# Kernel optimization log

Hardware: AMD Instinct MI355X
Metric: run time of the kernel (lower is better)

## Reference

```python
import jax, jax.numpy as jnp
import numpy as np

B, N, F_TOT, F_OBS = 64, 128, 80, 64
TAU, THRESH, EPS = 1.0, 0.5, 1e-8


def setup_inputs() -> dict:
    key = jax.random.key(0)
    k1, k2 = jax.random.split(key)
    h = jax.random.normal(k1, (B, N, F_TOT), dtype=jnp.float32)
    # xavier_uniform with gain=1.414 for a_link of shape (F_OBS, 1)
    bound = 1.414 * np.sqrt(6.0 / (F_OBS + 1))
    a_link = jax.random.uniform(k2, (F_OBS, 1), dtype=jnp.float32, minval=-bound, maxval=bound)
    return {"h": h, "a_link": a_link, "rollout": 1}


def reference(h, a_link, rollout):
    # h is detached in the original forward
    h_obs = jax.lax.stop_gradient(h[:, :, :F_OBS])            # [B, N, F_OBS]
    # pairwise |h_i - h_j| projected to a scalar logit per edge
    diff = jnp.abs(h_obs[:, :, None, :] - h_obs[:, None, :, :])  # [B, N, N, F_OBS]
    logits = jnp.einsum('bijk,kl->bijl', diff, a_link)[..., 0]   # [B, N, N]
    # gumbel_sigmoid with rollout=True: no noise, hard threshold + straight-through
    y_soft = jax.nn.sigmoid(logits / TAU)
    y_hard = (y_soft > THRESH).astype(y_soft.dtype)
    A = y_hard - jax.lax.stop_gradient(y_soft) + y_soft
    # log-likelihood of the sampled off-diagonal adjacency entries
    selected = A * y_soft + (1.0 - A) * (1.0 - y_soft)
    offdiag = 1.0 - jnp.eye(N, dtype=y_soft.dtype)              # [N, N]
    probs = jnp.sum(jnp.log(selected + EPS) * offdiag[None], axis=(1, 2))  # [B]
    # zero the diagonal of A, then add identity (self-loops forced to 1)
    A = A * offdiag[None] + jnp.eye(N, dtype=A.dtype)[None]
    return A, probs
```

## Files before the change

kernel.cpp:

```cpp
#include <hip/hip_runtime.h>

#define GB 64
#define GN 128
#define F_OBS 64
#define F_TOT 80
#define ISPLIT 32
#define IPB (GN / ISPLIT)

__global__ __launch_bounds__(128, 4) void glcn_main(
    const float* __restrict__ h, const float* __restrict__ w,
    float* __restrict__ Aout, float* __restrict__ part) {
  const int blk = blockIdx.x;
  const int b  = (blk & 7) + 8 * ((blk >> 3) & 7);
  const int q  = blk >> 6;
  const int is = q * IPB;
  const int j  = threadIdx.x;

  const float* rowj = h + ((size_t)(b * GN + j)) * F_TOT;
  const float* rows = h + ((size_t)(b * GN + is)) * F_TOT;

  float4 hj[F_OBS / 4];
#pragma unroll
  for (int kq = 0; kq < F_OBS / 4; ++kq)
    hj[kq] = *reinterpret_cast<const float4*>(rowj + 4 * kq);

  float acc[IPB];
#pragma unroll
  for (int ii = 0; ii < IPB; ++ii) acc[ii] = 0.f;

#pragma unroll
  for (int kq = 0; kq < F_OBS / 4; ++kq) {
    const float4 hv = hj[kq];
    const float4 wv = *reinterpret_cast<const float4*>(w + 4 * kq);
#pragma unroll
    for (int ii = 0; ii < IPB; ++ii) {
      const float* ri = rows + ii * F_TOT + 4 * kq;
      acc[ii] = fmaf(wv.x, fabsf(hv.x - ri[0]), acc[ii]);
      acc[ii] = fmaf(wv.y, fabsf(hv.y - ri[1]), acc[ii]);
      acc[ii] = fmaf(wv.z, fabsf(hv.z - ri[2]), acc[ii]);
      acc[ii] = fmaf(wv.w, fabsf(hv.w - ri[3]), acc[ii]);
    }
  }

  float logsum = 0.f;
  float* Abase = Aout + (size_t)b * GN * GN;
#pragma unroll
  for (int ii = 0; ii < IPB; ++ii) {
    const int i = is + ii;
    const float x = acc[ii];
    const float lt = -__logf(1.f + __expf(-fabsf(x)));
    float Aval = (x > 0.f) ? 1.f : 0.f;
    if (i == j) Aval = 1.f;
    else        logsum += lt;
    Abase[(size_t)i * GN + j] = Aval;
  }

#pragma unroll
  for (int off = 32; off > 0; off >>= 1)
    logsum += __shfl_down(logsum, off, 64);
  __shared__ float red[2];
  const int lane = threadIdx.x & 63;
  const int wid  = threadIdx.x >> 6;
  if (lane == 0) red[wid] = logsum;
  __syncthreads();
  if (threadIdx.x == 0) part[q * GB + b] = red[0] + red[1];
}

__global__ __launch_bounds__(64) void glcn_reduce(
    const float* __restrict__ part, float* __restrict__ probs) {
  const int b = threadIdx.x;
  float s = 0.f;
#pragma unroll
  for (int q = 0; q < ISPLIT; ++q) s += part[q * GB + b];
  probs[b] = s;
}

extern "C" void kernel_launch(void* const* d_in, const int* in_sizes, int n_in,
                              void* d_out, int out_size, void* d_ws, size_t ws_size,
                              hipStream_t stream) {
  const float* h = (const float*)d_in[0];
  const float* w = (const float*)d_in[1];
  float* Aout  = (float*)d_out;
  float* probs = Aout + (size_t)GB * GN * GN;
  float* part  = (float*)d_ws;

  glcn_main<<<GB * ISPLIT, 128, 0, stream>>>(h, w, Aout, part);
  glcn_reduce<<<1, 64, 0, stream>>>(part, probs);
}
```

Measured before the change: 14.47 us.

## Use 256-thread blocks, product-then-log, and drop shared-memory reduction

Blocks grow to 256 threads, with two 128-thread groups each covering 4 rows, so there are 1024 blocks instead of 2048 and 8 rows per block. The per-edge log is replaced by a product of (1+exp(-|x|)) terms followed by a single log per thread. Each wavefront writes its own partial sum, which removes the shared-memory stage and __syncthreads, and the reduce kernel now sums 64 slices. Multiplying four factors, each at most 2, cannot overflow, but the product-then-log form changes float rounding slightly.

```diff
diff --git a/kernel.cpp b/kernel.cpp
--- a/kernel.cpp
+++ b/kernel.cpp
@@ -4,17 +4,20 @@
 #define GN 128
 #define F_OBS 64
 #define F_TOT 80
-#define ISPLIT 32
-#define IPB (GN / ISPLIT)
+#define NBLK 1024
+#define NT 256
+#define IPT 4
 
-__global__ __launch_bounds__(128, 4) void glcn_main(
+__global__ __launch_bounds__(NT, 4) void glcn_main(
     const float* __restrict__ h, const float* __restrict__ w,
     float* __restrict__ Aout, float* __restrict__ part) {
   const int blk = blockIdx.x;
-  const int b  = (blk & 7) + 8 * ((blk >> 3) & 7);
-  const int q  = blk >> 6;
-  const int is = q * IPB;
-  const int j  = threadIdx.x;
+  const int b   = (blk & 7) + 8 * ((blk >> 3) & 7);
+  const int qq  = blk >> 6;
+  const int tid = threadIdx.x;
+  const int j   = tid & (GN - 1);
+  const int g   = __builtin_amdgcn_readfirstlane(tid >> 7);
+  const int is  = qq * 8 + g * IPT;
 
   const float* rowj = h + ((size_t)(b * GN + j)) * F_TOT;
   const float* rows = h + ((size_t)(b * GN + is)) * F_TOT;
@@ -24,16 +27,16 @@
   for (int kq = 0; kq < F_OBS / 4; ++kq)
     hj[kq] = *reinterpret_cast<const float4*>(rowj + 4 * kq);
 
-  float acc[IPB];
+  float acc[IPT];
 #pragma unroll
-  for (int ii = 0; ii < IPB; ++ii) acc[ii] = 0.f;
+  for (int ii = 0; ii < IPT; ++ii) acc[ii] = 0.f;
 
 #pragma unroll
   for (int kq = 0; kq < F_OBS / 4; ++kq) {
     const float4 hv = hj[kq];
     const float4 wv = *reinterpret_cast<const float4*>(w + 4 * kq);
 #pragma unroll
-    for (int ii = 0; ii < IPB; ++ii) {
+    for (int ii = 0; ii < IPT; ++ii) {
       const float* ri = rows + ii * F_TOT + 4 * kq;
       acc[ii] = fmaf(wv.x, fabsf(hv.x - ri[0]), acc[ii]);
       acc[ii] = fmaf(wv.y, fabsf(hv.y - ri[1]), acc[ii]);
@@ -42,28 +45,28 @@
     }
   }
 
-  float logsum = 0.f;
+  float prod = 1.f;
   float* Abase = Aout + (size_t)b * GN * GN;
 #pragma unroll
-  for (int ii = 0; ii < IPB; ++ii) {
+  for (int ii = 0; ii < IPT; ++ii) {
     const int i = is + ii;
     const float x = acc[ii];
-    const float lt = -__logf(1.f + __expf(-fabsf(x)));
+    const float f = 1.f + __expf(-fabsf(x));
     float Aval = (x > 0.f) ? 1.f : 0.f;
     if (i == j) Aval = 1.f;
-    else        logsum += lt;
+    else        prod *= f;
     Abase[(size_t)i * GN + j] = Aval;
   }
+  float lsum = -__logf(prod);
 
 #pragma unroll
   for (int off = 32; off > 0; off >>= 1)
-    logsum += __shfl_down(logsum, off, 64);
-  __shared__ float red[2];
-  const int lane = threadIdx.x & 63;
-  const int wid  = threadIdx.x >> 6;
-  if (lane == 0) red[wid] = logsum;
-  __syncthreads();
-  if (threadIdx.x == 0) part[q * GB + b] = red[0] + red[1];
+    lsum += __shfl_down(lsum, off, 64);
+  const int wid = tid >> 6;
+  if ((tid & 63) == 0) {
+    const int slice = qq * 4 + wid;
+    part[(size_t)slice * GB + b] = lsum;
+  }
 }
 
 __global__ __launch_bounds__(64) void glcn_reduce(
@@ -71,7 +74,7 @@
   const int b = threadIdx.x;
   float s = 0.f;
 #pragma unroll
-  for (int q = 0; q < ISPLIT; ++q) s += part[q * GB + b];
+  for (int q = 0; q < 64; ++q) s += part[(size_t)q * GB + b];
   probs[b] = s;
 }
 
@@ -84,6 +87,6 @@
   float* probs = Aout + (size_t)GB * GN * GN;
   float* part  = (float*)d_ws;
 
-  glcn_main<<<GB * ISPLIT, 128, 0, stream>>>(h, w, Aout, part);
+  glcn_main<<<NBLK, NT, 0, stream>>>(h, w, Aout, part);
   glcn_reduce<<<1, 64, 0, stream>>>(part, probs);
 }
```

New measurement: 14.29 us (median of 2 runs). No clear change (-1.2%).
